# Optimization experiments

Measured on AMD Instinct MI355X. Metric: run time of the kernel, lower is better.

Reference implementation:

```python
import jax, jax.numpy as jnp
import numpy as np

B, M, F, E = 64, 1024, 4, 256      # batch, memory length, tokens-per-memory-cell, emb_size
NW, HOPS, PL = 32000, 3, 128       # vocab, hops, profile_len


def _embed(table, idx):
    # nn.Embedding with padding_idx=0 -> index 0 maps to zero vector
    return table[idx] * (idx != 0)[..., None].astype(table.dtype)


def _gru_step(x, h, Wih, Whh, bih, bhh):
    # single-step PyTorch GRU cell
    gi = x @ Wih.T + bih
    gh = h @ Whh.T + bhh
    ir, iz, i_n = jnp.split(gi, 3, axis=-1)
    hr, hz, h_n = jnp.split(gh, 3, axis=-1)
    r = jax.nn.sigmoid(ir + hr)
    z = jax.nn.sigmoid(iz + hz)
    n = jnp.tanh(i_n + r * h_n)
    return (1.0 - z) * n + z * h


def setup_inputs() -> dict:
    key = jax.random.key(0)
    ks = jax.random.split(key, 13)
    # HOPS+1 unique embedding tables: A[0..hops-1] plus C[hops-1]; C[h]=tables[h+1] (weight tying)
    tables = (jax.random.normal(ks[0], (HOPS + 1, NW, E)) * 0.1).at[:, 0, :].set(0.0)
    s = 1.0 / np.sqrt(E)
    Wih = jax.random.uniform(ks[1], (3 * E, E), minval=-s, maxval=s)
    Whh = jax.random.uniform(ks[2], (3 * E, E), minval=-s, maxval=s)
    bih = jax.random.uniform(ks[3], (3 * E,), minval=-s, maxval=s)
    bhh = jax.random.uniform(ks[4], (3 * E,), minval=-s, maxval=s)
    sp = 1.0 / np.sqrt(PL)
    Wp = jax.random.uniform(ks[5], (E, PL), minval=-sp, maxval=sp)
    bp = jax.random.uniform(ks[6], (E,), minval=-sp, maxval=sp)
    sv = 1.0 / np.sqrt(2 * E)
    Wv = jax.random.uniform(ks[7], (NW, 2 * E), minval=-sv, maxval=sv)
    bv = jax.random.uniform(ks[8], (NW,), minval=-sv, maxval=sv)
    context = jax.random.randint(ks[9], (B, M, F), 0, NW)
    y_ = jax.random.randint(ks[10], (B,), 0, NW)
    h_ = jax.random.normal(ks[11], (1, B, E))
    profile_encoding = jax.random.normal(ks[12], (B, PL))
    return dict(tables=tables, Wih=Wih, Whh=Whh, bih=bih, bhh=bhh, Wp=Wp, bp=bp,
                Wv=Wv, bv=bv, context=context, y_=y_, h_=h_,
                profile_encoding=profile_encoding)


def reference(tables, Wih, Whh, bih, bhh, Wp, bp, Wv, bv, context, y_, h_, profile_encoding):
    # load_memory (eval mode: no word dropout): memories[h] = sum over F of table[h] embeddings
    ctx = context.reshape(B, M * F)
    mems = [_embed(tables[hop], ctx).reshape(B, M, F, E).sum(axis=2) for hop in range(HOPS + 1)]
    # decoder step
    m = _embed(tables[1], y_)                    # C[0](y_)
    h = _gru_step(m, h_[0], Wih, Whh, bih, bhh)  # [B, E]
    q = h
    p = p_vocab = p_resto = None
    for hop in range(HOPS):
        p_ = mems[hop] * q[:, None, :]           # [B, M, E] elementwise attention scores
        p = p_.sum(axis=2)                        # [B, M]
        attn = jax.nn.softmax(p, axis=1)
        o = jnp.einsum('bm,bme->be', attn, mems[hop + 1])
        if hop == 0:
            p_vocab = jnp.concatenate([h, o], axis=1) @ Wv.T + bv  # uses q[0]=h
        if hop == 1:
            enc = profile_encoding @ Wp.T + bp   # [B, E]
            p_resto = jnp.einsum('bme,be->bm', p_, enc)
        q = q + o
    return p, p_vocab, p_resto, h[None]          # p_ptr, p_vocab, p_resto, h [1,B,E]
```

## Files before the change

### kernel.cpp

```cpp
#include <hip/hip_runtime.h>
#include <cstdint>

#define B_ 64
#define M_ 1024
#define F_ 4
#define E_ 256
#define NW_ 32000
#define PL_ 128

#define P_OFF   0
#define PV_OFF  65536
#define PR_OFF  2113536
#define H_OFF   2179072

typedef unsigned short u16;
typedef unsigned int u32;

typedef __bf16 bf16x8 __attribute__((ext_vector_type(8)));
typedef float f32x4 __attribute__((ext_vector_type(4)));

__device__ __forceinline__ u16 f2bf(float f) {
    u32 x = __builtin_bit_cast(u32, f);
    u32 r = (x + 0x7fffu + ((x >> 16) & 1u)) >> 16;
    return (u16)r;
}
__device__ __forceinline__ float bf2f(u16 h) {
    return __builtin_bit_cast(float, (u32)h << 16);
}
__device__ __forceinline__ uint4 pack8(const float* s) {
    uint4 u;
    u.x = (u32)f2bf(s[0]) | ((u32)f2bf(s[1]) << 16);
    u.y = (u32)f2bf(s[2]) | ((u32)f2bf(s[3]) << 16);
    u.z = (u32)f2bf(s[4]) | ((u32)f2bf(s[5]) << 16);
    u.w = (u32)f2bf(s[6]) | ((u32)f2bf(s[7]) << 16);
    return u;
}
__device__ __forceinline__ bf16x8 pack_bf8(float4 a, float4 b) {
    union { u16 s[8]; bf16x8 v; } u;
    u.s[0] = f2bf(a.x); u.s[1] = f2bf(a.y); u.s[2] = f2bf(a.z); u.s[3] = f2bf(a.w);
    u.s[4] = f2bf(b.x); u.s[5] = f2bf(b.y); u.s[6] = f2bf(b.z); u.s[7] = f2bf(b.w);
    return u.v;
}

__global__ __launch_bounds__(256) void k_gru(
    const float* __restrict__ tables, const float* __restrict__ Wih,
    const float* __restrict__ Whh, const float* __restrict__ bih,
    const float* __restrict__ bhh, const float* __restrict__ Wp,
    const float* __restrict__ bp, const int* __restrict__ y,
    const float* __restrict__ h_, const float* __restrict__ pe,
    float* __restrict__ q0, float* __restrict__ q1, float* __restrict__ q2,
    float* __restrict__ enc, float* __restrict__ outh, u16* __restrict__ Qc0)
{
    int b = blockIdx.x, t = threadIdx.x;
    __shared__ float m_s[E_], h_s[E_], pe_s[PL_];
    int yb = y[b];
    m_s[t] = tables[(size_t)NW_ * E_ + (size_t)yb * E_ + t];
    h_s[t] = h_[b * E_ + t];
    if (t < PL_) pe_s[t] = pe[b * PL_ + t];
    __syncthreads();

    float g_i[3], g_h[3];
#pragma unroll
    for (int g = 0; g < 3; g++) {
        int j = g * E_ + t;
        float ai = bih[j], ah = bhh[j];
        const float4* wi = (const float4*)(Wih + (size_t)j * E_);
        const float4* wh = (const float4*)(Whh + (size_t)j * E_);
#pragma unroll 8
        for (int e = 0; e < E_ / 4; e++) {
            float4 a = wi[e], c = wh[e];
            ai += a.x * m_s[4 * e] + a.y * m_s[4 * e + 1] +
                  a.z * m_s[4 * e + 2] + a.w * m_s[4 * e + 3];
            ah += c.x * h_s[4 * e] + c.y * h_s[4 * e + 1] +
                  c.z * h_s[4 * e + 2] + c.w * h_s[4 * e + 3];
        }
        g_i[g] = ai; g_h[g] = ah;
    }
    float r = 1.f / (1.f + expf(-(g_i[0] + g_h[0])));
    float z = 1.f / (1.f + expf(-(g_i[1] + g_h[1])));
    float n = tanhf(g_i[2] + r * g_h[2]);
    float hv = (1.f - z) * n + z * h_s[t];
    q0[b * E_ + t] = hv;
    q1[b * E_ + t] = hv;
    q2[b * E_ + t] = hv;
    outh[b * E_ + t] = hv;
    u16 hi = f2bf(hv);
    Qc0[(size_t)b * E_ + t] = hi;
    Qc0[(size_t)(B_ + b) * E_ + t] = f2bf(hv - bf2f(hi));

    float ea = bp[t];
    const float4* wp = (const float4*)(Wp + (size_t)t * PL_);
#pragma unroll 8
    for (int p = 0; p < PL_ / 4; p++) {
        float4 a = wp[p];
        ea += a.x * pe_s[4 * p] + a.y * pe_s[4 * p + 1] +
              a.z * pe_s[4 * p + 2] + a.w * pe_s[4 * p + 3];
    }
    enc[b * E_ + t] = ea;
}

template <int WE>
__global__ __launch_bounds__(256) void k_qprep(
    const float* __restrict__ qsrc, const float* __restrict__ enc,
    u16* __restrict__ Qc)
{
    int b = blockIdx.x, t = threadIdx.x;
    float v = qsrc[b * E_ + t];
    u16 hi = f2bf(v);
    Qc[(size_t)b * E_ + t] = hi;
    Qc[(size_t)(B_ + b) * E_ + t] = f2bf(v - bf2f(hi));
    if (WE) {
        float e = v * enc[b * E_ + t];
        u16 h2 = f2bf(e);
        Qc[(size_t)(2 * B_ + b) * E_ + t] = h2;
        Qc[(size_t)(3 * B_ + b) * E_ + t] = f2bf(e - bf2f(h2));
    }
}

template <int NQ>
__global__ __launch_bounds__(256) void k_sgemm(
    const float* __restrict__ T, const u16* __restrict__ Qc,
    float* __restrict__ OA, float* __restrict__ OB)
{
    constexpr int NT = NQ * 4;
    __shared__ float lds[64][65];
    int t = threadIdx.x, lane = t & 63, wv = t >> 6;
    int l15 = lane & 15, quad = lane >> 4;
    int w0 = blockIdx.x * 64;
    const float* arow = T + (size_t)(w0 + wv * 16 + l15) * E_;
    f32x4 acc[NT];
#pragma unroll
    for (int nt = 0; nt < NT; nt++) acc[nt] = f32x4{0.f, 0.f, 0.f, 0.f};
#pragma unroll
    for (int ks = 0; ks < 8; ks++) {
        int k0 = ks * 32 + quad * 8;
        float4 a0 = *(const float4*)(arow + k0);
        float4 a1 = *(const float4*)(arow + k0 + 4);
        bf16x8 af = pack_bf8(a0, a1);
#pragma unroll
        for (int nt = 0; nt < NT; nt++) {
            bf16x8 bfr = *(const bf16x8*)(Qc + (size_t)(nt * 16 + l15) * E_ + k0);
            acc[nt] = __builtin_amdgcn_mfma_f32_16x16x32_bf16(af, bfr, acc[nt], 0, 0, 0);
        }
    }
#pragma unroll
    for (int arr = 0; arr < NQ / 2; arr++) {
        float* O = arr ? OB : OA;
        if (arr) __syncthreads();
#pragma unroll
        for (int nt = 0; nt < 4; nt++)
#pragma unroll
            for (int j = 0; j < 4; j++)
                lds[wv * 16 + quad * 4 + j][nt * 16 + l15] =
                    acc[arr * 8 + nt][j] + acc[arr * 8 + nt + 4][j];
        __syncthreads();
        int bb = t >> 2, ws = (t & 3) * 16;
        float vv[16];
#pragma unroll
        for (int i = 0; i < 16; i++) vv[i] = lds[ws + i][bb];
        float* orow = O + (size_t)bb * NW_ + w0 + ws;
        *(float4*)(orow)      = make_float4(vv[0], vv[1], vv[2], vv[3]);
        *(float4*)(orow + 4)  = make_float4(vv[4], vv[5], vv[6], vv[7]);
        *(float4*)(orow + 8)  = make_float4(vv[8], vv[9], vv[10], vv[11]);
        *(float4*)(orow + 12) = make_float4(vv[12], vv[13], vv[14], vv[15]);
    }
}

template <int MODE>
__global__ __launch_bounds__(256) void k_gsm(
    const float* __restrict__ S, const float* __restrict__ SR,
    const int* __restrict__ ctx, float* __restrict__ attn,
    float* __restrict__ outpr)
{
    int b = blockIdx.x, t = threadIdx.x;
    const float* Sb = S + (size_t)b * NW_;
    const int4* cp = (const int4*)(ctx + ((size_t)b * M_ + t * 4) * F_);
    int4 c0 = cp[0], c1 = cp[1], c2 = cp[2], c3 = cp[3];
    float p0 = Sb[c0.x] + Sb[c0.y] + Sb[c0.z] + Sb[c0.w];
    float p1 = Sb[c1.x] + Sb[c1.y] + Sb[c1.z] + Sb[c1.w];
    float p2 = Sb[c2.x] + Sb[c2.y] + Sb[c2.z] + Sb[c2.w];
    float p3 = Sb[c3.x] + Sb[c3.y] + Sb[c3.z] + Sb[c3.w];
    if constexpr (MODE == 1) {
        const float* Rb = SR + (size_t)b * NW_;
        float r0 = Rb[c0.x] + Rb[c0.y] + Rb[c0.z] + Rb[c0.w];
        float r1 = Rb[c1.x] + Rb[c1.y] + Rb[c1.z] + Rb[c1.w];
        float r2 = Rb[c2.x] + Rb[c2.y] + Rb[c2.z] + Rb[c2.w];
        float r3 = Rb[c3.x] + Rb[c3.y] + Rb[c3.z] + Rb[c3.w];
        *(float4*)(outpr + PR_OFF + (size_t)b * M_ + t * 4) =
            make_float4(r0, r1, r2, r3);
    }
    __shared__ float red[256];
    float lm = fmaxf(fmaxf(p0, p1), fmaxf(p2, p3));
    red[t] = lm;
    __syncthreads();
    for (int s = 128; s > 0; s >>= 1) {
        if (t < s) red[t] = fmaxf(red[t], red[t + s]);
        __syncthreads();
    }
    float mx = red[0];
    __syncthreads();
    float e0 = expf(p0 - mx), e1 = expf(p1 - mx);
    float e2 = expf(p2 - mx), e3 = expf(p3 - mx);
    red[t] = e0 + e1 + e2 + e3;
    __syncthreads();
    for (int s = 128; s > 0; s >>= 1) {
        if (t < s) red[t] += red[t + s];
        __syncthreads();
    }
    float inv = 1.f / red[0];
    *(float4*)(attn + (size_t)b * M_ + t * 4) =
        make_float4(e0 * inv, e1 * inv, e2 * inv, e3 * inv);
}

__global__ __launch_bounds__(256) void k_g2(
    const float* __restrict__ S, const int* __restrict__ ctx,
    float* __restrict__ out)
{
    int b = blockIdx.y;
    int m = blockIdx.x * 256 + threadIdx.x;
    const float* Sb = S + (size_t)b * NW_;
    int4 c = *(const int4*)(ctx + ((size_t)b * M_ + m) * F_);
    out[P_OFF + (size_t)b * M_ + m] = Sb[c.x] + Sb[c.y] + Sb[c.z] + Sb[c.w];
}

template <int NADD>
__global__ __launch_bounds__(256) void k_oacc(
    const float* __restrict__ T, const int* __restrict__ ctx,
    const float* __restrict__ attn, float* __restrict__ qa,
    float* __restrict__ qb)
{
    int b = blockIdx.y, chv = blockIdx.x, t = threadIdx.x;
    int m0 = chv * 128;
    __shared__ int cidx[512];
    __shared__ float aw[128];
    if (t < 128) aw[t] = attn[(size_t)b * M_ + m0 + t];
    ((int2*)cidx)[t] = ((const int2*)(ctx + ((size_t)b * M_ + m0) * F_))[t];
    __syncthreads();
    float acc0 = 0.f, acc1 = 0.f;
#pragma unroll 8
    for (int r = 0; r < 512; r += 2) {
        acc0 += aw[r >> 2]       * T[(size_t)cidx[r] * E_ + t];
        acc1 += aw[(r + 1) >> 2] * T[(size_t)cidx[r + 1] * E_ + t];
    }
    float acc = acc0 + acc1;
    atomicAdd(qa + b * E_ + t, acc);
    if constexpr (NADD == 2) atomicAdd(qb + b * E_ + t, acc);
}

__global__ __launch_bounds__(256) void k_pvocab(
    const float* __restrict__ Wv, const float* __restrict__ bv,
    const float* __restrict__ q0, const float* __restrict__ q1,
    float* __restrict__ out)
{
    __shared__ u16 X[64 * 512];
    int t = threadIdx.x;
#pragma unroll
    for (int it = 0; it < 16; it++) {
        int id = t + it * 256;
        int bb = id >> 6, c = id & 63;
        float v[8];
        if (c < 32) {
            const float* s = q0 + bb * E_ + c * 8;
#pragma unroll
            for (int j = 0; j < 8; j++) v[j] = s[j];
        } else {
            const float* s1 = q1 + bb * E_ + (c - 32) * 8;
            const float* s0 = q0 + bb * E_ + (c - 32) * 8;
#pragma unroll
            for (int j = 0; j < 8; j++) v[j] = s1[j] - s0[j];
        }
        uint4 uv = pack8(v);
        *(uint4*)(&X[bb * 512 + ((c ^ (bb & 7)) << 3)]) = uv;
    }
    __syncthreads();

    int lane = t & 63, w = t >> 6;
    int n0 = blockIdx.x * 128 + w * 32;
    int l15 = lane & 15, quad = lane >> 4;
    f32x4 acc[4][2];
#pragma unroll
    for (int mt = 0; mt < 4; mt++)
#pragma unroll
        for (int nt = 0; nt < 2; nt++)
            acc[mt][nt] = f32x4{0.f, 0.f, 0.f, 0.f};

    for (int ks = 0; ks < 16; ks++) {
        bf16x8 a[4], bfr[2];
#pragma unroll
        for (int mt = 0; mt < 4; mt++) {
            int m = mt * 16 + l15;
            int c = ks * 4 + quad;
            a[mt] = *(const bf16x8*)(&X[m * 512 + ((c ^ (m & 7)) << 3)]);
        }
#pragma unroll
        for (int nt = 0; nt < 2; nt++) {
            int n = n0 + nt * 16 + l15;
            const float4* wp = (const float4*)(Wv + (size_t)n * 512 + ks * 32 + quad * 8);
            bfr[nt] = pack_bf8(wp[0], wp[1]);
        }
#pragma unroll
        for (int mt = 0; mt < 4; mt++)
#pragma unroll
            for (int nt = 0; nt < 2; nt++)
                acc[mt][nt] = __builtin_amdgcn_mfma_f32_16x16x32_bf16(
                    a[mt], bfr[nt], acc[mt][nt], 0, 0, 0);
    }
#pragma unroll
    for (int nt = 0; nt < 2; nt++) {
        int n = n0 + nt * 16 + l15;
        float bvv = bv[n];
#pragma unroll
        for (int mt = 0; mt < 4; mt++) {
#pragma unroll
            for (int j = 0; j < 4; j++) {
                int m = mt * 16 + quad * 4 + j;
                out[PV_OFF + (size_t)m * 32000 + n] = acc[mt][nt][j] + bvv;
            }
        }
    }
}

extern "C" void kernel_launch(void* const* d_in, const int* in_sizes, int n_in,
                              void* d_out, int out_size, void* d_ws, size_t ws_size,
                              hipStream_t stream)
{
    const float* tables = (const float*)d_in[0];
    const float* Wih = (const float*)d_in[1];
    const float* Whh = (const float*)d_in[2];
    const float* bih = (const float*)d_in[3];
    const float* bhh = (const float*)d_in[4];
    const float* Wp  = (const float*)d_in[5];
    const float* bp  = (const float*)d_in[6];
    const float* Wv  = (const float*)d_in[7];
    const float* bv  = (const float*)d_in[8];
    const int* ctx = (const int*)d_in[9];
    const int* y   = (const int*)d_in[10];
    const float* h_  = (const float*)d_in[11];
    const float* pe  = (const float*)d_in[12];
    float* out = (float*)d_out;

    float* Wf   = (float*)d_ws;
    float* q0v  = Wf;
    float* q1v  = Wf + 16384;
    float* q2v  = Wf + 32768;
    float* encv = Wf + 49152;
    float* attn = Wf + 65536;
    u16* Qc0 = (u16*)(Wf + 131072);
    u16* Qc1 = Qc0 + 32768;
    u16* Qc2 = Qc1 + 65536;
    float* S0 = (float*)(Qc2 + 32768);
    float* S1 = S0 + (size_t)B_ * NW_;
    float* SRb = S1 + (size_t)B_ * NW_;
    float* S2 = SRb + (size_t)B_ * NW_;
    const float* T0 = tables;
    const float* T1 = tables + (size_t)NW_ * E_;
    const float* T2 = tables + 2 * (size_t)NW_ * E_;

    k_gru<<<64, 256, 0, stream>>>(tables, Wih, Whh, bih, bhh, Wp, bp, y, h_, pe,
                                  q0v, q1v, q2v, encv, out + H_OFF, Qc0);
    k_sgemm<2><<<500, 256, 0, stream>>>(T0, Qc0, S0, nullptr);
    k_gsm<0><<<64, 256, 0, stream>>>(S0, nullptr, ctx, attn, nullptr);
    k_oacc<2><<<dim3(8, 64), 256, 0, stream>>>(T1, ctx, attn, q1v, q2v);
    k_qprep<1><<<64, 256, 0, stream>>>(q1v, encv, Qc1);
    k_sgemm<4><<<500, 256, 0, stream>>>(T1, Qc1, S1, SRb);
    k_gsm<1><<<64, 256, 0, stream>>>(S1, SRb, ctx, attn, out);
    k_oacc<1><<<dim3(8, 64), 256, 0, stream>>>(T2, ctx, attn, q2v, nullptr);
    k_qprep<0><<<64, 256, 0, stream>>>(q2v, nullptr, Qc2);
    k_sgemm<2><<<500, 256, 0, stream>>>(T2, Qc2, S2, nullptr);
    k_g2<<<dim3(4, 64), 256, 0, stream>>>(S2, ctx, out);
    k_pvocab<<<250, 256, 0, stream>>>(Wv, bv, q0v, q1v, out);
}
```

Baseline: 461.0 us.

## Replace gathered attention readout with dense vocab-weight scatter and table sweep

The attention-weighted sum over gathered memory embeddings becomes two steps. Attention weights are scatter-added into a per-batch vocabulary histogram, then a dense pass streams each embedding table once, multiplying it by the histogram into per-chunk partial sums that the q-prep kernel reduces. This swaps about 262K random row gathers per hop for a sequential read of the full table, at the cost of atomics, zeroing a 64x32000 buffer and extra partial-sum traffic. The sgemm and pvocab kernels also get load prefetch batching and a retiled grid with 500 blocks.

```diff
diff --git a/kernel.cpp b/kernel.cpp
--- a/kernel.cpp
+++ b/kernel.cpp
@@ -12,6 +12,9 @@
 #define PV_OFF  65536
 #define PR_OFF  2113536
 #define H_OFF   2179072
+
+#define NCH_ 500
+#define WCH_ 64
 
 typedef unsigned short u16;
 typedef unsigned int u32;
@@ -48,8 +51,8 @@
     const float* __restrict__ bhh, const float* __restrict__ Wp,
     const float* __restrict__ bp, const int* __restrict__ y,
     const float* __restrict__ h_, const float* __restrict__ pe,
-    float* __restrict__ q0, float* __restrict__ q1, float* __restrict__ q2,
-    float* __restrict__ enc, float* __restrict__ outh, u16* __restrict__ Qc0)
+    float* __restrict__ q0, float* __restrict__ enc,
+    float* __restrict__ outh, u16* __restrict__ Qc0)
 {
     int b = blockIdx.x, t = threadIdx.x;
     __shared__ float m_s[E_], h_s[E_], pe_s[PL_];
@@ -81,8 +84,6 @@
     float n = tanhf(g_i[2] + r * g_h[2]);
     float hv = (1.f - z) * n + z * h_s[t];
     q0[b * E_ + t] = hv;
-    q1[b * E_ + t] = hv;
-    q2[b * E_ + t] = hv;
     outh[b * E_ + t] = hv;
     u16 hi = f2bf(hv);
     Qc0[(size_t)b * E_ + t] = hi;
@@ -101,19 +102,32 @@
 
 template <int WE>
 __global__ __launch_bounds__(256) void k_qprep(
-    const float* __restrict__ qsrc, const float* __restrict__ enc,
+    const float* __restrict__ qbase, const float* __restrict__ enc,
+    const float* __restrict__ opart, float* __restrict__ qout,
     u16* __restrict__ Qc)
 {
-    int b = blockIdx.x, t = threadIdx.x;
-    float v = qsrc[b * E_ + t];
-    u16 hi = f2bf(v);
-    Qc[(size_t)b * E_ + t] = hi;
-    Qc[(size_t)(B_ + b) * E_ + t] = f2bf(v - bf2f(hi));
-    if (WE) {
-        float e = v * enc[b * E_ + t];
-        u16 h2 = f2bf(e);
-        Qc[(size_t)(2 * B_ + b) * E_ + t] = h2;
-        Qc[(size_t)(3 * B_ + b) * E_ + t] = f2bf(e - bf2f(h2));
+    int b = blockIdx.x >> 2, eq = blockIdx.x & 3;
+    int t = threadIdx.x, sub = t >> 6, l = t & 63;
+    int e = eq * 64 + l;
+    float s = 0.f;
+#pragma unroll 5
+    for (int c = sub; c < NCH_; c += 4)
+        s += opart[((size_t)c * B_ + b) * E_ + e];
+    __shared__ float red[4][64];
+    red[sub][l] = s;
+    __syncthreads();
+    if (sub == 0) {
+        float v = qbase[b * E_ + e] + red[0][l] + red[1][l] + red[2][l] + red[3][l];
+        qout[b * E_ + e] = v;
+        u16 hi = f2bf(v);
+        Qc[(size_t)b * E_ + e] = hi;
+        Qc[(size_t)(B_ + b) * E_ + e] = f2bf(v - bf2f(hi));
+        if (WE) {
+            float ev = v * enc[b * E_ + e];
+            u16 h2 = f2bf(ev);
+            Qc[(size_t)(2 * B_ + b) * E_ + e] = h2;
+            Qc[(size_t)(3 * B_ + b) * E_ + e] = f2bf(ev - bf2f(h2));
+        }
     }
 }
 
@@ -123,6 +137,7 @@
     float* __restrict__ OA, float* __restrict__ OB)
 {
     constexpr int NT = NQ * 4;
+    constexpr int PF = (NQ == 2) ? 8 : 4;
     __shared__ float lds[64][65];
     int t = threadIdx.x, lane = t & 63, wv = t >> 6;
     int l15 = lane & 15, quad = lane >> 4;
@@ -131,16 +146,25 @@
     f32x4 acc[NT];
 #pragma unroll
     for (int nt = 0; nt < NT; nt++) acc[nt] = f32x4{0.f, 0.f, 0.f, 0.f};
-#pragma unroll
-    for (int ks = 0; ks < 8; ks++) {
-        int k0 = ks * 32 + quad * 8;
-        float4 a0 = *(const float4*)(arow + k0);
-        float4 a1 = *(const float4*)(arow + k0 + 4);
-        bf16x8 af = pack_bf8(a0, a1);
-#pragma unroll
-        for (int nt = 0; nt < NT; nt++) {
-            bf16x8 bfr = *(const bf16x8*)(Qc + (size_t)(nt * 16 + l15) * E_ + k0);
-            acc[nt] = __builtin_amdgcn_mfma_f32_16x16x32_bf16(af, bfr, acc[nt], 0, 0, 0);
+
+#pragma unroll
+    for (int g = 0; g < 8 / PF; g++) {
+        float4 a[PF][2];
+#pragma unroll
+        for (int k = 0; k < PF; k++) {
+            int k0 = (g * PF + k) * 32 + quad * 8;
+            a[k][0] = *(const float4*)(arow + k0);
+            a[k][1] = *(const float4*)(arow + k0 + 4);
+        }
+#pragma unroll
+        for (int k = 0; k < PF; k++) {
+            int k0 = (g * PF + k) * 32 + quad * 8;
+            bf16x8 af = pack_bf8(a[k][0], a[k][1]);
+#pragma unroll
+            for (int nt = 0; nt < NT; nt++) {
+                bf16x8 bfr = *(const bf16x8*)(Qc + (size_t)(nt * 16 + l15) * E_ + k0);
+                acc[nt] = __builtin_amdgcn_mfma_f32_16x16x32_bf16(af, bfr, acc[nt], 0, 0, 0);
+            }
         }
     }
 #pragma unroll
@@ -169,10 +193,14 @@
 template <int MODE>
 __global__ __launch_bounds__(256) void k_gsm(
     const float* __restrict__ S, const float* __restrict__ SR,
-    const int* __restrict__ ctx, float* __restrict__ attn,
+    const int* __restrict__ ctx, float* __restrict__ wgt,
     float* __restrict__ outpr)
 {
     int b = blockIdx.x, t = threadIdx.x;
+    float* Wb = wgt + (size_t)b * NW_;
+#pragma unroll 5
+    for (int i = 0; i < NW_ / 256; i++) Wb[i * 256 + t] = 0.f;
+
     const float* Sb = S + (size_t)b * NW_;
     const int4* cp = (const int4*)(ctx + ((size_t)b * M_ + t * 4) * F_);
     int4 c0 = cp[0], c1 = cp[1], c2 = cp[2], c3 = cp[3];
@@ -208,8 +236,54 @@
         __syncthreads();
     }
     float inv = 1.f / red[0];
-    *(float4*)(attn + (size_t)b * M_ + t * 4) =
-        make_float4(e0 * inv, e1 * inv, e2 * inv, e3 * inv);
+    float a0 = e0 * inv, a1 = e1 * inv, a2 = e2 * inv, a3 = e3 * inv;
+    atomicAdd(Wb + c0.x, a0); atomicAdd(Wb + c0.y, a0);
+    atomicAdd(Wb + c0.z, a0); atomicAdd(Wb + c0.w, a0);
+    atomicAdd(Wb + c1.x, a1); atomicAdd(Wb + c1.y, a1);
+    atomicAdd(Wb + c1.z, a1); atomicAdd(Wb + c1.w, a1);
+    atomicAdd(Wb + c2.x, a2); atomicAdd(Wb + c2.y, a2);
+    atomicAdd(Wb + c2.z, a2); atomicAdd(Wb + c2.w, a2);
+    atomicAdd(Wb + c3.x, a3); atomicAdd(Wb + c3.y, a3);
+    atomicAdd(Wb + c3.z, a3); atomicAdd(Wb + c3.w, a3);
+}
+
+__global__ __launch_bounds__(256) void k_odense(
+    const float* __restrict__ T, const float* __restrict__ wgt,
+    float* __restrict__ opart)
+{
+    int ch = blockIdx.x, t = threadIdx.x;
+    int w0 = ch * WCH_;
+    __shared__ float wg_s[B_][WCH_ + 4];
+    {
+        int bb = t >> 2, seg = (t & 3) * 16;
+        const float* src = wgt + (size_t)bb * NW_ + w0 + seg;
+        float4 v0 = *(const float4*)(src);
+        float4 v1 = *(const float4*)(src + 4);
+        float4 v2 = *(const float4*)(src + 8);
+        float4 v3 = *(const float4*)(src + 12);
+        *(float4*)&wg_s[bb][seg]      = v0;
+        *(float4*)&wg_s[bb][seg + 4]  = v1;
+        *(float4*)&wg_s[bb][seg + 8]  = v2;
+        *(float4*)&wg_s[bb][seg + 12] = v3;
+    }
+    __syncthreads();
+    float acc[B_];
+#pragma unroll
+    for (int b = 0; b < B_; b++) acc[b] = 0.f;
+    for (int wq = 0; wq < WCH_ / 4; wq++) {
+        float t0 = T[(size_t)(w0 + 4 * wq + 0) * E_ + t];
+        float t1 = T[(size_t)(w0 + 4 * wq + 1) * E_ + t];
+        float t2 = T[(size_t)(w0 + 4 * wq + 2) * E_ + t];
+        float t3 = T[(size_t)(w0 + 4 * wq + 3) * E_ + t];
+#pragma unroll
+        for (int b = 0; b < B_; b++) {
+            float4 wv = *(const float4*)&wg_s[b][4 * wq];
+            acc[b] += wv.x * t0 + wv.y * t1 + wv.z * t2 + wv.w * t3;
+        }
+    }
+#pragma unroll
+    for (int b = 0; b < B_; b++)
+        opart[((size_t)ch * B_ + b) * E_ + t] = acc[b];
 }
 
 __global__ __launch_bounds__(256) void k_g2(
@@ -221,30 +295,6 @@
     const float* Sb = S + (size_t)b * NW_;
     int4 c = *(const int4*)(ctx + ((size_t)b * M_ + m) * F_);
     out[P_OFF + (size_t)b * M_ + m] = Sb[c.x] + Sb[c.y] + Sb[c.z] + Sb[c.w];
-}
-
-template <int NADD>
-__global__ __launch_bounds__(256) void k_oacc(
-    const float* __restrict__ T, const int* __restrict__ ctx,
-    const float* __restrict__ attn, float* __restrict__ qa,
-    float* __restrict__ qb)
-{
-    int b = blockIdx.y, chv = blockIdx.x, t = threadIdx.x;
-    int m0 = chv * 128;
-    __shared__ int cidx[512];
-    __shared__ float aw[128];
-    if (t < 128) aw[t] = attn[(size_t)b * M_ + m0 + t];
-    ((int2*)cidx)[t] = ((const int2*)(ctx + ((size_t)b * M_ + m0) * F_))[t];
-    __syncthreads();
-    float acc0 = 0.f, acc1 = 0.f;
-#pragma unroll 8
-    for (int r = 0; r < 512; r += 2) {
-        acc0 += aw[r >> 2]       * T[(size_t)cidx[r] * E_ + t];
-        acc1 += aw[(r + 1) >> 2] * T[(size_t)cidx[r + 1] * E_ + t];
-    }
-    float acc = acc0 + acc1;
-    atomicAdd(qa + b * E_ + t, acc);
-    if constexpr (NADD == 2) atomicAdd(qb + b * E_ + t, acc);
 }
 
 __global__ __launch_bounds__(256) void k_pvocab(
@@ -275,47 +325,42 @@
     __syncthreads();
 
     int lane = t & 63, w = t >> 6;
-    int n0 = blockIdx.x * 128 + w * 32;
     int l15 = lane & 15, quad = lane >> 4;
-    f32x4 acc[4][2];
-#pragma unroll
-    for (int mt = 0; mt < 4; mt++)
-#pragma unroll
-        for (int nt = 0; nt < 2; nt++)
-            acc[mt][nt] = f32x4{0.f, 0.f, 0.f, 0.f};
-
-    for (int ks = 0; ks < 16; ks++) {
-        bf16x8 a[4], bfr[2];
-#pragma unroll
-        for (int mt = 0; mt < 4; mt++) {
-            int m = mt * 16 + l15;
-            int c = ks * 4 + quad;
-            a[mt] = *(const bf16x8*)(&X[m * 512 + ((c ^ (m & 7)) << 3)]);
-        }
-#pragma unroll
-        for (int nt = 0; nt < 2; nt++) {
-            int n = n0 + nt * 16 + l15;
-            const float4* wp = (const float4*)(Wv + (size_t)n * 512 + ks * 32 + quad * 8);
-            bfr[nt] = pack_bf8(wp[0], wp[1]);
-        }
-#pragma unroll
-        for (int mt = 0; mt < 4; mt++)
-#pragma unroll
-            for (int nt = 0; nt < 2; nt++)
-                acc[mt][nt] = __builtin_amdgcn_mfma_f32_16x16x32_bf16(
-                    a[mt], bfr[nt], acc[mt][nt], 0, 0, 0);
-    }
-#pragma unroll
-    for (int nt = 0; nt < 2; nt++) {
-        int n = n0 + nt * 16 + l15;
-        float bvv = bv[n];
-#pragma unroll
-        for (int mt = 0; mt < 4; mt++) {
-#pragma unroll
-            for (int j = 0; j < 4; j++) {
-                int m = mt * 16 + quad * 4 + j;
-                out[PV_OFF + (size_t)m * 32000 + n] = acc[mt][nt][j] + bvv;
+    int n = blockIdx.x * 64 + w * 16 + l15;
+    const float4* wp = (const float4*)(Wv + (size_t)n * 512);
+    f32x4 acc[4];
+#pragma unroll
+    for (int mt = 0; mt < 4; mt++) acc[mt] = f32x4{0.f, 0.f, 0.f, 0.f};
+
+#pragma unroll
+    for (int half = 0; half < 2; half++) {
+        float4 wv[8][2];
+#pragma unroll
+        for (int k8 = 0; k8 < 8; k8++) {
+            int ks = half * 8 + k8;
+            wv[k8][0] = wp[ks * 8 + quad * 2];
+            wv[k8][1] = wp[ks * 8 + quad * 2 + 1];
+        }
+#pragma unroll
+        for (int k8 = 0; k8 < 8; k8++) {
+            int ks = half * 8 + k8;
+            bf16x8 bfr = pack_bf8(wv[k8][0], wv[k8][1]);
+#pragma unroll
+            for (int mt = 0; mt < 4; mt++) {
+                int m = mt * 16 + l15;
+                int c = ks * 4 + quad;
+                bf16x8 a = *(const bf16x8*)(&X[m * 512 + ((c ^ (m & 7)) << 3)]);
+                acc[mt] = __builtin_amdgcn_mfma_f32_16x16x32_bf16(a, bfr, acc[mt], 0, 0, 0);
             }
+        }
+    }
+    float bvv = bv[n];
+#pragma unroll
+    for (int mt = 0; mt < 4; mt++) {
+#pragma unroll
+        for (int j = 0; j < 4; j++) {
+            int m = mt * 16 + quad * 4 + j;
+            out[PV_OFF + (size_t)m * 32000 + n] = acc[mt][j] + bvv;
         }
     }
 }
@@ -344,29 +389,30 @@
     float* q1v  = Wf + 16384;
     float* q2v  = Wf + 32768;
     float* encv = Wf + 49152;
-    float* attn = Wf + 65536;
-    u16* Qc0 = (u16*)(Wf + 131072);
+    u16* Qc0 = (u16*)(Wf + 65536);
     u16* Qc1 = Qc0 + 32768;
     u16* Qc2 = Qc1 + 65536;
-    float* S0 = (float*)(Qc2 + 32768);
+    float* S0 = Wf + 131072;
     float* S1 = S0 + (size_t)B_ * NW_;
     float* SRb = S1 + (size_t)B_ * NW_;
     float* S2 = SRb + (size_t)B_ * NW_;
+    float* wgt = S2 + (size_t)B_ * NW_;
+    float* opart = wgt + (size_t)B_ * NW_;
     const float* T0 = tables;
     const float* T1 = tables + (size_t)NW_ * E_;
     const float* T2 = tables + 2 * (size_t)NW_ * E_;
 
     k_gru<<<64, 256, 0, stream>>>(tables, Wih, Whh, bih, bhh, Wp, bp, y, h_, pe,
-                                  q0v, q1v, q2v, encv, out + H_OFF, Qc0);
+                                  q0v, encv, out + H_OFF, Qc0);
     k_sgemm<2><<<500, 256, 0, stream>>>(T0, Qc0, S0, nullptr);
-    k_gsm<0><<<64, 256, 0, stream>>>(S0, nullptr, ctx, attn, nullptr);
-    k_oacc<2><<<dim3(8, 64), 256, 0, stream>>>(T1, ctx, attn, q1v, q2v);
-    k_qprep<1><<<64, 256, 0, stream>>>(q1v, encv, Qc1);
+    k_gsm<0><<<64, 256, 0, stream>>>(S0, nullptr, ctx, wgt, nullptr);
+    k_odense<<<NCH_, 256, 0, stream>>>(T1, wgt, opart);
+    k_qprep<1><<<256, 256, 0, stream>>>(q0v, encv, opart, q1v, Qc1);
     k_sgemm<4><<<500, 256, 0, stream>>>(T1, Qc1, S1, SRb);
-    k_gsm<1><<<64, 256, 0, stream>>>(S1, SRb, ctx, attn, out);
-    k_oacc<1><<<dim3(8, 64), 256, 0, stream>>>(T2, ctx, attn, q2v, nullptr);
-    k_qprep<0><<<64, 256, 0, stream>>>(q2v, nullptr, Qc2);
+    k_gsm<1><<<64, 256, 0, stream>>>(S1, SRb, ctx, wgt, out);
+    k_odense<<<NCH_, 256, 0, stream>>>(T2, wgt, opart);
+    k_qprep<0><<<256, 256, 0, stream>>>(q1v, nullptr, opart, q2v, Qc2);
     k_sgemm<2><<<500, 256, 0, stream>>>(T2, Qc2, S2, nullptr);
     k_g2<<<dim3(4, 64), 256, 0, stream>>>(S2, ctx, out);
-    k_pvocab<<<250, 256, 0, stream>>>(Wv, bv, q0v, q1v, out);
-}
+    k_pvocab<<<500, 256, 0, stream>>>(Wv, bv, q0v, q1v, out);
+}
```

After: 514.8 us. +11.7%, slower.
